# Kernel tuning notes

Measured on AMD Instinct MI355X. Metric: run time of the kernel, lower is better.

## Reference

```python
import jax, jax.numpy as jnp
import numpy as np
from jax import lax

# Architecture constants (match init_kwargs)
B = 4          # clips
T_SEG = 8      # num_segments
D_IN = 256
D_HID = 64
H = 112
W = 112
WIN_T = 5      # window[0], temporal
WIN_S = 9      # window[1] == window[2], spatial
MAXD = WIN_S // 2


def setup_inputs() -> dict:
    key = jax.random.key(0)
    k1, k2, k3, k4 = jax.random.split(key, 4)
    x = jax.random.normal(k1, (B * T_SEG, D_IN, H, W), jnp.float32)
    conv_w = jax.random.normal(k2, (D_HID, D_IN, 3, 3), jnp.float32) * 0.05
    bn_gamma = jnp.ones((D_HID,), jnp.float32)
    bn_beta = jnp.zeros((D_HID,), jnp.float32)
    bn_mean = jax.random.normal(k3, (D_HID,), jnp.float32) * 0.1
    bn_var = jax.random.uniform(k4, (D_HID,), jnp.float32, minval=0.5, maxval=1.5)
    return {"x": x, "conv_w": conv_w, "bn_gamma": bn_gamma, "bn_beta": bn_beta,
            "bn_mean": bn_mean, "bn_var": bn_var}


def reference(x, conv_w, bn_gamma, bn_beta, bn_mean, bn_var):
    # downsample: Conv2d(k=3, s=2, p=1, no bias) + BatchNorm2d (eval) + ReLU
    y = lax.conv_general_dilated(x, conv_w, window_strides=(2, 2),
                                 padding=((1, 1), (1, 1)),
                                 dimension_numbers=("NCHW", "OIHW", "NCHW"))
    scale = bn_gamma / jnp.sqrt(bn_var + 1e-5)
    y = jax.nn.relu((y - bn_mean[:, None, None]) * scale[:, None, None]
                    + bn_beta[:, None, None])
    bt, c, h, w = y.shape
    b = bt // T_SEG
    y = y.reshape(b, T_SEG, c, h, w)
    # per-frame, per-pixel L2 normalization over channels (eps=1e-6, as in _L2normalize)
    yn = y / jnp.sqrt(jnp.sum(y * y, axis=2, keepdims=True) + 1e-6)
    # temporal zero-pad (padded frames normalize to 0 in the original too: 0/sqrt(eps)=0)
    half_t = WIN_T // 2
    ypad = jnp.pad(yn, ((0, 0), (half_t, half_t), (0, 0), (0, 0), (0, 0)))
    # spatial zero-pad by max displacement
    ypad = jnp.pad(ypad, ((0, 0), (0, 0), (0, 0), (MAXD, MAXD), (MAXD, MAXD)))
    # temporal windows: f2[b, t, l] = padded frame t+l   -> (b, T, L, c, h+2m, w+2m)
    f2 = jnp.stack([ypad[:, l:l + T_SEG] for l in range(WIN_T)], axis=2)
    # local windowed correlation (equivalent to einsum + _corr_abs_to_rel):
    # out[b,t,l,u,v,h,w] = sum_c yn[b,t,c,h,w] * f2[b,t,l,c,h+u,w+v]
    corrs = []
    for u in range(WIN_S):
        for v in range(WIN_S):
            corrs.append(jnp.einsum("btchw,btlchw->btlhw",
                                     yn, f2[:, :, :, :, u:u + h, v:v + w]))
    corr = jnp.stack(corrs, axis=-1).reshape(b, T_SEG, WIN_T, h, w, WIN_S, WIN_S)
    # '(b t l) u v h w -> b t h w 1 l u v'
    corr = jnp.transpose(corr, (0, 1, 3, 4, 2, 5, 6))
    return corr[:, :, :, :, None, :, :, :]
```

## Files before the change

kernel.cpp:

```cpp
#include <hip/hip_runtime.h>
#include <hip/hip_bf16.h>

#define TSEG 8
#define NBC 4
#define NBT 32
#define CIN 256
#define CH 64
#define HIN 112
#define WIN_ 112
#define HO 56
#define WO 56
#define HPD 64
#define WPD 64

#define FRSZE ((size_t)(HPD * WPD * CH))
#define ZF_U   147456
#define FR_U   (ZF_U + 262144)
#define WS_TOTAL_BYTES ((size_t)(FR_U + 32 * 262144) * 2)

typedef __attribute__((ext_vector_type(8))) short bf16x8;
typedef __attribute__((ext_vector_type(4))) float f32x4;

__device__ __forceinline__ unsigned short f2bf(float f) {
    union { float f; unsigned u; } c; c.f = f;
    unsigned u = c.u + 0x7fffu + ((c.u >> 16) & 1u);
    return (unsigned short)(u >> 16);
}

__global__ __launch_bounds__(256) void wprep_k(
    const float* __restrict__ w, unsigned short* __restrict__ wpp)
{
    int e = blockIdx.x * 256 + threadIdx.x;
    int cout = e / 2304;
    int rem  = e - cout * 2304;
    int ci   = rem / 9;
    int tap  = rem - ci * 9;
    wpp[((size_t)tap * 64 + cout) * 256 + ci] = f2bf(w[e]);
}

__global__ __launch_bounds__(256) void conv_mfma_k(
    const float* __restrict__ x, const unsigned short* __restrict__ wpp,
    const float* __restrict__ gamma, const float* __restrict__ beta,
    const float* __restrict__ mean, const float* __restrict__ var,
    unsigned short* __restrict__ frames)
{
    __shared__ unsigned short in_lds[5 * 120 * 32];
    __shared__ float sq[2][2][64];

    const int tid  = threadIdx.x;
    const int lane = tid & 63;
    const int wv   = tid >> 6;
    const int r    = wv >> 1;
    const int nh   = wv & 1;
    const int l15  = lane & 15;
    const int l4   = lane >> 4;
    const int hb   = blockIdx.x;
    const int bt   = blockIdx.y;

    const float* xb = x + (size_t)bt * (CIN * HIN * WIN_);

    f32x4 acc[4][2];
#pragma unroll
    for (int mt = 0; mt < 4; ++mt) {
        acc[mt][0] = (f32x4){0.f, 0.f, 0.f, 0.f};
        acc[mt][1] = (f32x4){0.f, 0.f, 0.f, 0.f};
    }

    int a_off[4][3];
#pragma unroll
    for (int mt = 0; mt < 4; ++mt) {
        int c = mt * 16 + l15; if (c > 55) c = 55;
#pragma unroll
        for (int kw = 0; kw < 3; ++kw) {
            int col = 2 * c + kw;
            int ba  = col * 64 + l4 * 16;
            ba ^= ((col >> 1) & 7) << 4;
            a_off[mt][kw] = ba;
        }
    }

    const unsigned short* bptr0 = wpp + ((size_t)(nh * 32 + l15) * 256 + l4 * 8);
    const unsigned short* bptr1 = wpp + ((size_t)(nh * 32 + 16 + l15) * 256 + l4 * 8);

    const int ih0 = 4 * hb - 1;

    for (int cb = 0; cb < 8; ++cb) {
        __syncthreads();
#pragma unroll
        for (int j = 0; j < 5; ++j) {
            const int jj  = wv + j * 4;
            const int row = jj >> 2, cig = jj & 3;
            const int ih  = ih0 + row;
            const int ihc = ih < 0 ? 0 : (ih > 111 ? 111 : ih);
            const float* xr = xb + ((size_t)(cb * 32 + cig * 8) * HIN + ihc) * WIN_;
            const bool rowin = (ih >= 0) && (ih < HIN);
#pragma unroll
            for (int p = 0; p < 2; ++p) {
                const int col = lane + p * 64;
                if (col < 113) {
                    const int iw  = col - 1;
                    const int iwc = iw < 0 ? 0 : iw;
                    const bool inb = rowin && (iw >= 0);
                    unsigned pk[4];
#pragma unroll
                    for (int q = 0; q < 4; ++q) {
                        float v0 = xr[(size_t)(2 * q) * HIN * WIN_ + iwc];
                        float v1 = xr[(size_t)(2 * q + 1) * HIN * WIN_ + iwc];
                        v0 = inb ? v0 : 0.f;
                        v1 = inb ? v1 : 0.f;
                        union { float f; unsigned u; } c0, c1; c0.f = v0; c1.f = v1;
                        unsigned u0 = c0.u + 0x7fffu + ((c0.u >> 16) & 1u);
                        unsigned u1 = c1.u + 0x7fffu + ((c1.u >> 16) & 1u);
                        pk[q] = (u0 >> 16) | (u1 & 0xffff0000u);
                    }
                    int ba = (row * 120 + col) * 64 + cig * 16;
                    ba ^= ((col >> 1) & 7) << 4;
                    *(uint4*)((char*)in_lds + ba) = make_uint4(pk[0], pk[1], pk[2], pk[3]);
                }
            }
        }
        __syncthreads();

        const int rowb = (2 * r) * 7680;
#pragma unroll
        for (int kh = 0; kh < 3; ++kh) {
            const int rb = rowb + kh * 7680;
#pragma unroll
            for (int kw = 0; kw < 3; ++kw) {
                const int tap = kh * 3 + kw;
                const bf16x8 bf0 = *(const bf16x8*)(bptr0 + tap * 16384 + cb * 32);
                const bf16x8 bf1 = *(const bf16x8*)(bptr1 + tap * 16384 + cb * 32);
#pragma unroll
                for (int mt = 0; mt < 4; ++mt) {
                    const bf16x8 af = *(const bf16x8*)((const char*)in_lds + (rb + a_off[mt][kw]));
                    acc[mt][0] = __builtin_amdgcn_mfma_f32_16x16x32_bf16(af, bf0, acc[mt][0], 0, 0, 0);
                    acc[mt][1] = __builtin_amdgcn_mfma_f32_16x16x32_bf16(af, bf1, acc[mt][1], 0, 0, 0);
                }
            }
        }
    }

    const int cout0 = nh * 32 + l15;
    const int cout1 = cout0 + 16;
    const float sc0 = gamma[cout0] * rsqrtf(var[cout0] + 1e-5f);
    const float bb0 = beta[cout0] - mean[cout0] * sc0;
    const float sc1 = gamma[cout1] * rsqrtf(var[cout1] + 1e-5f);
    const float bb1 = beta[cout1] - mean[cout1] * sc1;

    float yv[4][2][4];
    float ssr[4][4];
#pragma unroll
    for (int mt = 0; mt < 4; ++mt) {
#pragma unroll
        for (int reg = 0; reg < 4; ++reg) {
            float y0 = fmaxf(fmaf(acc[mt][0][reg], sc0, bb0), 0.f);
            float y1 = fmaxf(fmaf(acc[mt][1][reg], sc1, bb1), 0.f);
            yv[mt][0][reg] = y0; yv[mt][1][reg] = y1;
            float ss = y0 * y0 + y1 * y1;
            ss += __shfl_xor(ss, 1);
            ss += __shfl_xor(ss, 2);
            ss += __shfl_xor(ss, 4);
            ss += __shfl_xor(ss, 8);
            ssr[mt][reg] = ss;
        }
    }
    if (l15 == 0) {
#pragma unroll
        for (int mt = 0; mt < 4; ++mt)
#pragma unroll
            for (int reg = 0; reg < 4; ++reg)
                sq[r][nh][mt * 16 + l4 * 4 + reg] = ssr[mt][reg];
    }
    __syncthreads();

    const int h = 2 * hb + r;
    unsigned short* fdst = frames + (size_t)bt * FRSZE + (size_t)(h + 4) * WPD * CH;
#pragma unroll
    for (int mt = 0; mt < 4; ++mt) {
#pragma unroll
        for (int reg = 0; reg < 4; ++reg) {
            const int c = mt * 16 + l4 * 4 + reg;
            if (c < 56) {
                const float tot = sq[r][0][c] + sq[r][1][c];
                const float inv = rsqrtf(tot + 1e-6f);
                unsigned short* dp = fdst + (size_t)(c + 4) * CH;
                dp[cout0] = f2bf(yv[mt][0][reg] * inv);
                dp[cout1] = f2bf(yv[mt][1][reg] * inv);
            }
        }
    }
}

__global__ __launch_bounds__(256) void corr_mfma_k(
    const unsigned short* __restrict__ frames, float* __restrict__ out)
{
    __shared__ float so[56 * 84];

    const int tid  = threadIdx.x;
    const int lane = tid & 63;
    const int wv   = tid >> 6;
    const int l15  = lane & 15;
    const int l4   = lane >> 4;
    const int h    = blockIdx.x;
    const int t    = blockIdx.y;
    const int b    = blockIdx.z;
    const int bt   = b * TSEG + t;

    const unsigned short* yrow = frames + (size_t)bt * FRSZE + (size_t)(h + 4) * (WPD * CH);
    bf16x8 af[4][2];
#pragma unroll
    for (int m = 0; m < 4; ++m) {
        int w = (m << 4) + l15; if (w > 55) w = 55;
        const unsigned short* ap = yrow + (size_t)(w + 4) * CH + (l4 << 3);
        af[m][0] = *(const bf16x8*)(ap);
        af[m][1] = *(const bf16x8*)(ap + 32);
    }

    float* obase = out + (size_t)(bt * HO + h) * (WO * 405);

    const int PM[7] = {0, 0, 1, 1, 2, 2, 3};
    const int PN[7] = {0, 1, 1, 2, 2, 3, 3};

    for (int l = 0; l < 5; ++l) {
        const int f = t + l;
        const bool isPad = (f < 2) || (f > 9);

        if (isPad) {
            for (int e = tid; e < 56 * 84; e += 256) so[e] = 0.f;
        } else {
            const unsigned short* fr = frames + (size_t)(b * TSEG + f - 2) * FRSZE;
            for (int u = wv; u < 9; u += 4) {
                const unsigned short* zrow = fr + (size_t)(h + u) * (WPD * CH);
                bf16x8 bfr[4][2];
#pragma unroll
                for (int n = 0; n < 4; ++n) {
                    const unsigned short* bp = zrow + (size_t)((n << 4) + l15) * CH + (l4 << 3);
                    bfr[n][0] = *(const bf16x8*)(bp);
                    bfr[n][1] = *(const bf16x8*)(bp + 32);
                }

                f32x4 acc[7];
#pragma unroll
                for (int i = 0; i < 7; ++i) acc[i] = (f32x4){0.f, 0.f, 0.f, 0.f};
#pragma unroll
                for (int i = 0; i < 7; ++i) {
                    acc[i] = __builtin_amdgcn_mfma_f32_16x16x32_bf16(af[PM[i]][0], bfr[PN[i]][0], acc[i], 0, 0, 0);
                    acc[i] = __builtin_amdgcn_mfma_f32_16x16x32_bf16(af[PM[i]][1], bfr[PN[i]][1], acc[i], 0, 0, 0);
                }

#pragma unroll
                for (int i = 0; i < 7; ++i) {
                    const int zc = (PN[i] << 4) + l15;
                    const int w0 = (PM[i] << 4) + (l4 << 2);
#pragma unroll
                    for (int rr = 0; rr < 4; ++rr) {
                        const int w = w0 + rr;
                        const int v = zc - w;
                        if (w < 56 && (unsigned)v <= 8u)
                            so[w * 84 + u * 9 + v] = acc[i][rr];
                    }
                }
            }
        }
        __syncthreads();

        float* ob = obase + l * 81;
#pragma unroll
        for (int ww = 0; ww < 14; ++ww) {
            const int w = wv * 14 + ww;
            const float* sr = so + w * 84;
            float* orow = ob + (size_t)w * 405;
            orow[lane] = sr[lane];
            if (lane < 17) orow[lane + 64] = sr[lane + 64];
        }
        __syncthreads();
    }
}

extern "C" void kernel_launch(void* const* d_in, const int* in_sizes, int n_in,
                              void* d_out, int out_size, void* d_ws, size_t ws_size,
                              hipStream_t stream)
{
    const float* x     = (const float*)d_in[0];
    const float* wgt   = (const float*)d_in[1];
    const float* gamma = (const float*)d_in[2];
    const float* beta  = (const float*)d_in[3];
    const float* mean  = (const float*)d_in[4];
    const float* var   = (const float*)d_in[5];
    float* out = (float*)d_out;

    unsigned short* wpp    = (unsigned short*)d_ws;
    unsigned short* frames = wpp + FR_U;

    if (ws_size < WS_TOTAL_BYTES) return;

    hipMemsetAsync(d_ws, 0, WS_TOTAL_BYTES, stream);
    wprep_k<<<dim3(576), 256, 0, stream>>>(wgt, wpp);
    conv_mfma_k<<<dim3(28, NBT), 256, 0, stream>>>(x, wpp, gamma, beta, mean, var, frames);
    corr_mfma_k<<<dim3(56, TSEG, NBC), 256, 0, stream>>>(frames, out);
}
```

Before: 305.4 us.

## Restructure correlation around source frame with LDS-staged swizzled window rows

Measured after the change: 278.5 us. 8.8% less time.

```diff
diff --git a/kernel.cpp b/kernel.cpp
--- a/kernel.cpp
+++ b/kernel.cpp
@@ -191,89 +191,128 @@
     }
 }
 
-__global__ __launch_bounds__(256) void corr_mfma_k(
+__global__ __launch_bounds__(64) void pad_k(float* __restrict__ out)
+{
+    const int lane = threadIdx.x;
+    const int h = blockIdx.x;
+    const int p = blockIdx.y;
+    const int b = blockIdx.z;
+    const int PT[6] = {0, 0, 1, 6, 7, 7};
+    const int PL[6] = {0, 1, 0, 4, 3, 4};
+    const int t = PT[p], l = PL[p];
+    float* ob = out + (size_t)((b * TSEG + t) * HO + h) * (WO * 405) + l * 81;
+#pragma unroll 4
+    for (int w = 0; w < 56; ++w) {
+        float* orow = ob + (size_t)w * 405;
+        orow[lane] = 0.f;
+        if (lane < 17) orow[lane + 64] = 0.f;
+    }
+}
+
+__global__ __launch_bounds__(256) void corr_f_k(
     const unsigned short* __restrict__ frames, float* __restrict__ out)
 {
-    __shared__ float so[56 * 84];
+    __shared__ unsigned short zl[9 * 4096];
+    __shared__ float so[4][504];
 
     const int tid  = threadIdx.x;
     const int lane = tid & 63;
     const int wv   = tid >> 6;
     const int l15  = lane & 15;
     const int l4   = lane >> 4;
-    const int h    = blockIdx.x;
-    const int t    = blockIdx.y;
-    const int b    = blockIdx.z;
-    const int bt   = b * TSEG + t;
-
-    const unsigned short* yrow = frames + (size_t)bt * FRSZE + (size_t)(h + 4) * (WPD * CH);
-    bf16x8 af[4][2];
-#pragma unroll
-    for (int m = 0; m < 4; ++m) {
-        int w = (m << 4) + l15; if (w > 55) w = 55;
-        const unsigned short* ap = yrow + (size_t)(w + 4) * CH + (l4 << 3);
-        af[m][0] = *(const bf16x8*)(ap);
-        af[m][1] = *(const bf16x8*)(ap + 32);
-    }
-
-    float* obase = out + (size_t)(bt * HO + h) * (WO * 405);
+    const int w7   = lane / 9;
+    const int v9   = lane - w7 * 9;
+
+    const int h = blockIdx.x;
+    const int f = blockIdx.y;
+    const int b = blockIdx.z;
+
+    const unsigned short* zb = frames + (size_t)(b * TSEG + f) * FRSZE
+                             + (size_t)h * (WPD * CH);
+#pragma unroll
+    for (int k = 0; k < 18; ++k) {
+        const int e   = tid + k * 256;
+        const int row = e >> 9;
+        const int c   = e & 511;
+        const uint4 val = *(const uint4*)(zb + (size_t)row * 4096 + c * 8);
+        const int ba = row * 8192 + ((c * 16) ^ (((c >> 3) & 7) << 4));
+        *(uint4*)((char*)zl + ba) = val;
+    }
+    __syncthreads();
+
+    int roff[4][2];
+#pragma unroll
+    for (int n = 0; n < 4; ++n) {
+        const int px = n * 16 + l15;
+#pragma unroll
+        for (int hf = 0; hf < 2; ++hf)
+            roff[n][hf] = (px * 128 + hf * 64 + l4 * 16) ^ ((px & 7) << 4);
+    }
 
     const int PM[7] = {0, 0, 1, 1, 2, 2, 3};
     const int PN[7] = {0, 1, 1, 2, 2, 3, 3};
-
-    for (int l = 0; l < 5; ++l) {
-        const int f = t + l;
-        const bool isPad = (f < 2) || (f > 9);
-
-        if (isPad) {
-            for (int e = tid; e < 56 * 84; e += 256) so[e] = 0.f;
-        } else {
-            const unsigned short* fr = frames + (size_t)(b * TSEG + f - 2) * FRSZE;
-            for (int u = wv; u < 9; u += 4) {
-                const unsigned short* zrow = fr + (size_t)(h + u) * (WPD * CH);
-                bf16x8 bfr[4][2];
-#pragma unroll
-                for (int n = 0; n < 4; ++n) {
-                    const unsigned short* bp = zrow + (size_t)((n << 4) + l15) * CH + (l4 << 3);
-                    bfr[n][0] = *(const bf16x8*)(bp);
-                    bfr[n][1] = *(const bf16x8*)(bp + 32);
+    float* sw = so[wv];
+
+    for (int pass = 0; pass < 2; ++pass) {
+        if (pass == 1 && wv != 0) break;
+        const int l = (pass == 0) ? wv : 4;
+        const int t = f + 2 - l;
+        if (t < 0 || t > 7) continue;
+        const int bt = b * TSEG + t;
+
+        const unsigned short* yb = frames + (size_t)bt * FRSZE
+                                 + (size_t)(h + 4) * (WPD * CH);
+        bf16x8 yf[4][2];
+#pragma unroll
+        for (int m = 0; m < 4; ++m) {
+            int wc = (m << 4) + l15; if (wc > 55) wc = 55;
+            const unsigned short* ap = yb + (size_t)(wc + 4) * CH + (l4 << 3);
+            yf[m][0] = *(const bf16x8*)(ap);
+            yf[m][1] = *(const bf16x8*)(ap + 32);
+        }
+
+        float* ob = out + (size_t)(bt * HO + h) * (WO * 405) + l * 81;
+
+#pragma unroll
+        for (int u = 0; u < 9; ++u) {
+            const char* rb = (const char*)zl + u * 8192;
+            bf16x8 zf[4][2];
+#pragma unroll
+            for (int n = 0; n < 4; ++n) {
+                zf[n][0] = *(const bf16x8*)(rb + roff[n][0]);
+                zf[n][1] = *(const bf16x8*)(rb + roff[n][1]);
+            }
+
+            f32x4 acc[7];
+#pragma unroll
+            for (int i = 0; i < 7; ++i) acc[i] = (f32x4){0.f, 0.f, 0.f, 0.f};
+#pragma unroll
+            for (int i = 0; i < 7; ++i) {
+                acc[i] = __builtin_amdgcn_mfma_f32_16x16x32_bf16(zf[PN[i]][0], yf[PM[i]][0], acc[i], 0, 0, 0);
+                acc[i] = __builtin_amdgcn_mfma_f32_16x16x32_bf16(zf[PN[i]][1], yf[PM[i]][1], acc[i], 0, 0, 0);
+            }
+
+#pragma unroll
+            for (int i = 0; i < 7; ++i) {
+                const int w = (PM[i] << 4) + l15;
+#pragma unroll
+                for (int reg = 0; reg < 4; ++reg) {
+                    const int zc = (PN[i] << 4) + (l4 << 2) + reg;
+                    const int v  = zc - w;
+                    if (w < 56 && (unsigned)v <= 8u)
+                        sw[w * 9 + v] = acc[i][reg];
                 }
-
-                f32x4 acc[7];
-#pragma unroll
-                for (int i = 0; i < 7; ++i) acc[i] = (f32x4){0.f, 0.f, 0.f, 0.f};
-#pragma unroll
-                for (int i = 0; i < 7; ++i) {
-                    acc[i] = __builtin_amdgcn_mfma_f32_16x16x32_bf16(af[PM[i]][0], bfr[PN[i]][0], acc[i], 0, 0, 0);
-                    acc[i] = __builtin_amdgcn_mfma_f32_16x16x32_bf16(af[PM[i]][1], bfr[PN[i]][1], acc[i], 0, 0, 0);
+            }
+
+            if (w7 < 7) {
+                float* obu = ob + u * 9;
+#pragma unroll
+                for (int it = 0; it < 8; ++it) {
+                    const int w = it * 7 + w7;
+                    obu[(size_t)w * 405 + v9] = sw[w * 9 + v9];
                 }
-
-#pragma unroll
-                for (int i = 0; i < 7; ++i) {
-                    const int zc = (PN[i] << 4) + l15;
-                    const int w0 = (PM[i] << 4) + (l4 << 2);
-#pragma unroll
-                    for (int rr = 0; rr < 4; ++rr) {
-                        const int w = w0 + rr;
-                        const int v = zc - w;
-                        if (w < 56 && (unsigned)v <= 8u)
-                            so[w * 84 + u * 9 + v] = acc[i][rr];
-                    }
-                }
-            }
-        }
-        __syncthreads();
-
-        float* ob = obase + l * 81;
-#pragma unroll
-        for (int ww = 0; ww < 14; ++ww) {
-            const int w = wv * 14 + ww;
-            const float* sr = so + w * 84;
-            float* orow = ob + (size_t)w * 405;
-            orow[lane] = sr[lane];
-            if (lane < 17) orow[lane + 64] = sr[lane + 64];
-        }
-        __syncthreads();
+            }
+        }
     }
 }
 
@@ -297,5 +336,6 @@
     hipMemsetAsync(d_ws, 0, WS_TOTAL_BYTES, stream);
     wprep_k<<<dim3(576), 256, 0, stream>>>(wgt, wpp);
     conv_mfma_k<<<dim3(28, NBT), 256, 0, stream>>>(x, wpp, gamma, beta, mean, var, frames);
-    corr_mfma_k<<<dim3(56, TSEG, NBC), 256, 0, stream>>>(frames, out);
-}
+    pad_k<<<dim3(56, 6, NBC), 64, 0, stream>>>(out);
+    corr_f_k<<<dim3(56, TSEG, NBC), 256, 0, stream>>>(frames, out);
+}
```
